# Kernel tuning notes

Hardware: AMD Instinct MI355X
Metric: run time of the kernel (lower is better)

The kernel has to match this reference:

```python
import jax, jax.numpy as jnp
import numpy as np

N_RNA, N_DIS = 50000, 2000
E_RD = E_DR = E_RR = 200000
D_IN, D_DIS, C, H = 256, 128, 64, 4
HC = H * C  # heads * out_channels = 256
NEG_SLOPE = 0.2


def setup_inputs() -> dict:
    ks = jax.random.split(jax.random.key(0), 64)
    it = iter(range(64))
    def nrm(shape, s=0.05):
        return jax.random.normal(ks[next(it)], shape, jnp.float32) * s
    inp = {}
    inp["x_rna"] = nrm((N_RNA, D_IN), 1.0)
    inp["x_dis"] = nrm((N_DIS, D_DIS), 1.0)
    inp["w_rd"] = jax.random.uniform(ks[next(it)], (E_RD,), jnp.float32)
    inp["w_dr"] = jax.random.uniform(ks[next(it)], (E_DR,), jnp.float32)
    inp["w_rr"] = jax.random.uniform(ks[next(it)], (E_RR,), jnp.float32)
    inp["lin_d_W"] = nrm((D_DIS, D_IN)); inp["lin_d_b"] = nrm((D_IN,))
    for rel in ("rd", "dr", "rr"):
        inp[f"{rel}_Wl"]  = nrm((D_IN, HC))   # GATv2 lin_l (source)
        inp[f"{rel}_bl"]  = nrm((HC,))
        inp[f"{rel}_Wr"]  = nrm((D_IN, HC))   # GATv2 lin_r (target)
        inp[f"{rel}_br"]  = nrm((HC,))
        inp[f"{rel}_We"]  = nrm((1, HC))      # lin_edge (edge_dim=1, no bias)
        inp[f"{rel}_att"] = nrm((H, C))       # attention vector per head
        inp[f"{rel}_bias"] = nrm((HC,))       # conv output bias (concat heads)
    inp["lin_out_W"] = nrm((HC, C)); inp["lin_out_b"] = nrm((C,))
    inp["ei_rd_src"] = jax.random.randint(ks[next(it)], (E_RD,), 0, N_RNA)
    inp["ei_rd_dst"] = jax.random.randint(ks[next(it)], (E_RD,), 0, N_DIS)
    inp["ei_dr_src"] = jax.random.randint(ks[next(it)], (E_DR,), 0, N_DIS)
    inp["ei_dr_dst"] = jax.random.randint(ks[next(it)], (E_DR,), 0, N_RNA)
    inp["ei_rr_src"] = jax.random.randint(ks[next(it)], (E_RR,), 0, N_RNA)
    inp["ei_rr_dst"] = jax.random.randint(ks[next(it)], (E_RR,), 0, N_RNA)
    return inp


def _gatv2(x_src, x_dst, src, dst, w, Wl, bl, Wr, br, We, att, bias, n_dst):
    """GATv2Conv with edge_dim=1, add_self_loops=False, concat heads."""
    xl = (x_src @ Wl + bl).reshape(-1, H, C)              # [Ns,H,C]
    xr = (x_dst @ Wr + br).reshape(-1, H, C)              # [Nd,H,C]
    ew = (w[:, None] @ We).reshape(-1, H, C)              # [E,H,C]
    m = jax.nn.leaky_relu(xl[src] + xr[dst] + ew, NEG_SLOPE)
    alpha = jnp.einsum('ehc,hc->eh', m, att)              # [E,H]
    # segment softmax over edges sharing the same destination node
    amax = jax.ops.segment_max(alpha, dst, num_segments=n_dst)
    ex = jnp.exp(alpha - jax.lax.stop_gradient(amax)[dst])
    den = jax.ops.segment_sum(ex, dst, num_segments=n_dst)
    a = ex / (den[dst] + 1e-16)                           # [E,H]
    out = jax.ops.segment_sum(xl[src] * a[..., None], dst, num_segments=n_dst)
    return out.reshape(n_dst, HC) + bias                  # [n_dst, H*C]


def reference(x_rna, x_dis, w_rd, w_dr, w_rr, lin_d_W, lin_d_b,
              rd_Wl, rd_bl, rd_Wr, rd_br, rd_We, rd_att, rd_bias,
              dr_Wl, dr_bl, dr_Wr, dr_br, dr_We, dr_att, dr_bias,
              rr_Wl, rr_bl, rr_Wr, rr_br, rr_We, rr_att, rr_bias,
              lin_out_W, lin_out_b,
              ei_rd_src, ei_rd_dst, ei_dr_src, ei_dr_dst, ei_rr_src, ei_rr_dst):
    xd = x_dis @ lin_d_W + lin_d_b  # project disease feats to rna_in_dim
    h_dis = _gatv2(x_rna, xd, ei_rd_src, ei_rd_dst, w_rd,
                   rd_Wl, rd_bl, rd_Wr, rd_br, rd_We, rd_att, rd_bias, N_DIS)
    h_rna = (_gatv2(xd, x_rna, ei_dr_src, ei_dr_dst, w_dr,
                    dr_Wl, dr_bl, dr_Wr, dr_br, dr_We, dr_att, dr_bias, N_RNA)
             + _gatv2(x_rna, x_rna, ei_rr_src, ei_rr_dst, w_rr,
                      rr_Wl, rr_bl, rr_Wr, rr_br, rr_We, rr_att, rr_bias, N_RNA))
    h_rna = h_rna @ lin_out_W + lin_out_b
    h_dis = h_dis @ lin_out_W + lin_out_b
    return jnp.concatenate([h_rna, h_dis], axis=0)  # [N_RNA+N_DIS, C]
```

## Files before the change

kernel.cpp:

```cpp
#include <hip/hip_runtime.h>
#include <stdint.h>

#define NRNA 50000
#define NDIS 2000
#define NEDGE 200000
#define MP_RNA 50048
#define MP_DIS 2048
#define NOUT 52000
#define MP_OUT2 52096
#define SSTRIDE 50064

#define MAXD0 192
#define MAXD12 32
#define EPB0 0
#define EPB1 (NDIS * MAXD0)
#define EPB2 (EPB1 + NRNA * MAXD12)
#define EPTOT (EPB2 + NRNA * MAXD12)

#define GB_BIG 391
#define GB_SML 16
#define NFILL ((3 * NEDGE + 511) / 512)
#define SWZP 997LL

typedef __attribute__((ext_vector_type(4))) float f32x4;
typedef __attribute__((ext_vector_type(2))) float f32x2;
typedef __attribute__((ext_vector_type(8))) short s16x8;
typedef __attribute__((ext_vector_type(4))) unsigned short u16x4;

#define AS1C const __attribute__((address_space(1))) unsigned int*
#define AS3P __attribute__((address_space(3))) unsigned int*

static __device__ __forceinline__ unsigned short f2b(float f) {
  unsigned u = __float_as_uint(f);
  u += 0x7FFFu + ((u >> 16) & 1u);
  return (unsigned short)(u >> 16);
}
static __device__ __forceinline__ float b2f(unsigned short h) {
  return __uint_as_float(((unsigned)h) << 16);
}
static __device__ __forceinline__ f32x2 unpk2(unsigned u) {
  f32x2 r;
  r[0] = __uint_as_float(u << 16);
  r[1] = __uint_as_float(u & 0xFFFF0000u);
  return r;
}
static __device__ __forceinline__ f32x2 vabs2(f32x2 v) {
  f32x2 r;
  r[0] = __uint_as_float(__float_as_uint(v[0]) & 0x7FFFFFFFu);
  r[1] = __uint_as_float(__float_as_uint(v[1]) & 0x7FFFFFFFu);
  return r;
}

struct TcEnt { const float* W; unsigned short* WT; int K; int N; };
struct Prep {
  const float* xr; unsigned short* xrb;
  const float* xd; unsigned short* xdb;
  TcEnt tc[8];
};
#define PREP_C1 12512
#define PREP_C2 (PREP_C1 + 256)
__global__ __launch_bounds__(256) void k_prep(Prep pr) {
  int id = blockIdx.x;
  if (id < PREP_C1) {
    int idx = (id * 256 + threadIdx.x) * 4;
    int row = idx >> 8;
    u16x4 o;
    if (row < NRNA) {
      f32x4 v = *(const f32x4*)(pr.xr + idx);
      o[0] = f2b(v[0]); o[1] = f2b(v[1]); o[2] = f2b(v[2]); o[3] = f2b(v[3]);
    } else { o[0] = 0; o[1] = 0; o[2] = 0; o[3] = 0; }
    *(u16x4*)(pr.xrb + idx) = o;
  } else if (id < PREP_C2) {
    int idx = ((id - PREP_C1) * 256 + threadIdx.x) * 4;
    int row = idx >> 7;
    u16x4 o;
    if (row < NDIS) {
      f32x4 v = *(const f32x4*)(pr.xd + idx);
      o[0] = f2b(v[0]); o[1] = f2b(v[1]); o[2] = f2b(v[2]); o[3] = f2b(v[3]);
    } else { o[0] = 0; o[1] = 0; o[2] = 0; o[3] = 0; }
    *(u16x4*)(pr.xdb + idx) = o;
  } else {
    int e = (id - PREP_C2) >> 8;
    int idx = ((id - PREP_C2) & 255) * 256 + threadIdx.x;
    TcEnt t = pr.tc[e];
    if (idx < t.K * t.N) {
      int k = idx / t.N, n = idx - k * t.N;
      t.WT[n * t.K + k] = f2b(t.W[idx]);
    }
  }
}

template<int K, int N>
__global__ __launch_bounds__(256) void k_gemm(
    const unsigned short* __restrict__ A, const unsigned short* __restrict__ WT,
    const float* __restrict__ bias, unsigned short* __restrict__ Cb) {
  constexpr int NT = N / 16;
  int lane = threadIdx.x & 63;
  int wave = threadIdx.x >> 6;
  int row0 = blockIdx.x * 64 + wave * 16;
  int lr = lane & 15, kg = lane >> 4;
  f32x4 acc[NT];
#pragma unroll
  for (int i = 0; i < NT; i++) acc[i] = (f32x4)0.f;
  const unsigned short* arow = A + (size_t)(row0 + lr) * K + kg * 8;
#pragma unroll
  for (int kk = 0; kk < K; kk += 32) {
    s16x8 af = *(const s16x8*)(arow + kk);
#pragma unroll
    for (int nt = 0; nt < NT; nt++) {
      s16x8 bf = *(const s16x8*)(WT + (size_t)(nt * 16 + lr) * K + kk + kg * 8);
      acc[nt] = __builtin_amdgcn_mfma_f32_16x16x32_bf16(af, bf, acc[nt], 0, 0, 0);
    }
  }
#pragma unroll
  for (int nt = 0; nt < NT; nt++) {
    int col = nt * 16 + lr;
    float bb = bias[col];
#pragma unroll
    for (int r = 0; r < 4; r++) {
      int row = row0 + kg * 4 + r;
      Cb[(size_t)row * N + col] = f2b(acc[nt][r] + bb);
    }
  }
}

__device__ __forceinline__ void gemm256(const unsigned short* __restrict__ A,
    const unsigned short* __restrict__ WT, const float* __restrict__ bias,
    unsigned short* __restrict__ C, int bxx) {
  __shared__ unsigned short Alds[2][128 * 32];
  __shared__ unsigned short Blds[2][256 * 32];
  const int t = threadIdx.x;
  const int wid = t >> 6, lane = t & 63;
  const int lr = lane & 15, kg = lane >> 4;
  const int wr = wid & 3, wc = wid >> 2;
  const int r0 = bxx * 128;
  f32x4 acc[2][8];
#pragma unroll
  for (int a = 0; a < 2; a++)
#pragma unroll
    for (int b = 0; b < 8; b++) acc[a][b] = (f32x4)0.f;

  auto stage = [&](int buf, int ks) {
    __builtin_amdgcn_global_load_lds(
        (AS1C)(A + (size_t)(r0 + (t & 127)) * 256 + ks * 32 + (t >> 7) * 8),
        (AS3P)((char*)&Alds[buf][0] + t * 16), 16, 0, 0);
    __builtin_amdgcn_global_load_lds(
        (AS1C)(WT + (size_t)(t & 255) * 256 + ks * 32 + (t >> 8) * 8),
        (AS3P)((char*)&Blds[buf][0] + t * 16), 16, 0, 0);
    __builtin_amdgcn_global_load_lds(
        (AS1C)(WT + (size_t)(t & 255) * 256 + ks * 32 + ((t >> 8) + 2) * 8),
        (AS3P)((char*)&Blds[buf][0] + (t + 512) * 16), 16, 0, 0);
  };

  stage(0, 0);
  __syncthreads();
  for (int ks = 0; ks < 8; ++ks) {
    int cur = ks & 1;
    if (ks < 7) stage(cur ^ 1, ks + 1);
    s16x8 a0 = *(const s16x8*)&Alds[cur][(kg * 128 + wr * 32 + lr) * 8];
    s16x8 a1 = *(const s16x8*)&Alds[cur][(kg * 128 + wr * 32 + 16 + lr) * 8];
#pragma unroll
    for (int nt = 0; nt < 8; ++nt) {
      s16x8 bf = *(const s16x8*)&Blds[cur][(kg * 256 + wc * 128 + nt * 16 + lr) * 8];
      acc[0][nt] = __builtin_amdgcn_mfma_f32_16x16x32_bf16(a0, bf, acc[0][nt], 0, 0, 0);
      acc[1][nt] = __builtin_amdgcn_mfma_f32_16x16x32_bf16(a1, bf, acc[1][nt], 0, 0, 0);
    }
    __syncthreads();
  }
#pragma unroll
  for (int nt = 0; nt < 8; ++nt) {
    int col = wc * 128 + nt * 16 + lr;
    float bb = bias[col];
#pragma unroll
    for (int rt = 0; rt < 2; ++rt)
#pragma unroll
      for (int i = 0; i < 4; ++i) {
        int row = r0 + wr * 32 + rt * 16 + kg * 4 + i;
        C[(size_t)row * 256 + col] = f2b(acc[rt][nt][i] + bb);
      }
  }
}

struct MegaG {
  const unsigned short* A[6];
  const unsigned short* WT[6];
  const float* bias[6];
  unsigned short* C[6];
  int off[7];
  int nmega;
  const int* src[3]; const int* dst[3]; const float* w[3];
  int* cnt; unsigned* ep;
};
__global__ __launch_bounds__(512) void k_megaG(MegaG m) {
  int id = (int)(((long long)blockIdx.x * SWZP) % m.nmega);
  if (id < m.off[6]) {
    int sel = 0;
#pragma unroll
    for (int s = 1; s < 6; ++s) sel += (id >= m.off[s]);
    gemm256(m.A[sel], m.WT[sel], m.bias[sel], m.C[sel], id - m.off[sel]);
  } else {
    int i = (id - m.off[6]) * 512 + threadIdx.x;
    if (i < 3 * NEDGE) {
      int r = i / NEDGE;
      int e = i - r * NEDGE;
      int n = m.dst[r][e];
      int c = atomicAdd(&m.cnt[r * SSTRIDE + n], 1);
      int maxd = (r == 0) ? MAXD0 : MAXD12;
      int base = (r == 0) ? EPB0 : (r == 1) ? EPB1 : EPB2;
      if (c < maxd) {
        unsigned v = ((unsigned)f2b(m.w[r][e]) << 16) | (unsigned)m.src[r][e];
        m.ep[base + n * maxd + c] = v;
      }
    }
  }
}

struct G2S { const unsigned short* A; const unsigned short* WT[2];
             const float* b[2]; unsigned short* C[2]; };
__global__ __launch_bounds__(512) void k_gemmP(G2S g) {
  gemm256(g.A, g.WT[blockIdx.y], g.b[blockIdx.y], g.C[blockIdx.y], blockIdx.x);
}

__global__ __launch_bounds__(256) void k_gemmO(const unsigned short* __restrict__ A,
    const unsigned short* __restrict__ WT, const float* __restrict__ bias,
    float* __restrict__ Cf, int Mstore) {
  __shared__ unsigned short Alds[2][128 * 32];
  __shared__ unsigned short Blds[2][64 * 32];
  const int t = threadIdx.x;
  const int lane = t & 63, wid = t >> 6;
  const int lr = lane & 15, kg = lane >> 4;
  const int wr = wid;
  const int r0 = blockIdx.x * 128;
  f32x4 acc[2][4];
#pragma unroll
  for (int a = 0; a < 2; a++)
#pragma unroll
    for (int b = 0; b < 4; b++) acc[a][b] = (f32x4)0.f;
  auto stage = [&](int buf, int ks) {
    __builtin_amdgcn_global_load_lds(
        (AS1C)(A + (size_t)(r0 + (t & 127)) * 256 + ks * 32 + (t >> 7) * 8),
        (AS3P)((char*)&Alds[buf][0] + t * 16), 16, 0, 0);
    __builtin_amdgcn_global_load_lds(
        (AS1C)(A + (size_t)(r0 + (t & 127)) * 256 + ks * 32 + ((t >> 7) + 2) * 8),
        (AS3P)((char*)&Alds[buf][0] + (t + 256) * 16), 16, 0, 0);
    __builtin_amdgcn_global_load_lds(
        (AS1C)(WT + (size_t)(t & 63) * 256 + ks * 32 + (t >> 6) * 8),
        (AS3P)((char*)&Blds[buf][0] + t * 16), 16, 0, 0);
  };
  stage(0, 0);
  __syncthreads();
  for (int ks = 0; ks < 8; ++ks) {
    int cur = ks & 1;
    if (ks < 7) stage(cur ^ 1, ks + 1);
    s16x8 a0 = *(const s16x8*)&Alds[cur][(kg * 128 + wr * 32 + lr) * 8];
    s16x8 a1 = *(const s16x8*)&Alds[cur][(kg * 128 + wr * 32 + 16 + lr) * 8];
#pragma unroll
    for (int nt = 0; nt < 4; ++nt) {
      s16x8 bf = *(const s16x8*)&Blds[cur][(kg * 64 + nt * 16 + lr) * 8];
      acc[0][nt] = __builtin_amdgcn_mfma_f32_16x16x32_bf16(a0, bf, acc[0][nt], 0, 0, 0);
      acc[1][nt] = __builtin_amdgcn_mfma_f32_16x16x32_bf16(a1, bf, acc[1][nt], 0, 0, 0);
    }
    __syncthreads();
  }
#pragma unroll
  for (int nt = 0; nt < 4; ++nt) {
    int col = nt * 16 + lr;
    float bb = bias[col];
#pragma unroll
    for (int rt = 0; rt < 2; ++rt)
#pragma unroll
      for (int i = 0; i < 4; ++i) {
        int row = r0 + wr * 32 + rt * 16 + kg * 4 + i;
        if (row < Mstore) Cf[(size_t)row * 64 + col] = acc[rt][nt][i] + bb;
      }
  }
}

struct Agg {
  f32x2 we01, we23, a6_01, a4_01, a6_23, a4_23, xr01, xr23;
  const unsigned short* xlb;
  const unsigned* epn;
  float m, d;
  f32x2 o01, o23;

  __device__ __forceinline__ void init(const unsigned short* xl, const unsigned short* xr,
      const unsigned* ep_rel, int maxd, int node,
      const float* We, const float* att, int lane) {
    const f32x2* Wep = (const f32x2*)(We + lane * 4);
    we01 = Wep[0]; we23 = Wep[1];
    const f32x2* atp = (const f32x2*)(att + lane * 4);
    a6_01 = atp[0] * 0.6f; a4_01 = atp[0] * 0.4f;
    a6_23 = atp[1] * 0.6f; a4_23 = atp[1] * 0.4f;
    uint2 xruu = *(const uint2*)(xr + (size_t)node * 256 + lane * 4);
    xr01 = unpk2(xruu.x); xr23 = unpk2(xruu.y);
    xlb = xl + lane * 4;
    epn = ep_rel + node * maxd;
    m = -INFINITY; d = 0.f;
    o01 = (f32x2){0.f, 0.f}; o23 = (f32x2){0.f, 0.f};
  }

  __device__ __forceinline__ void batch4(int e, int deg) {
    int nb = deg - e; nb = (nb > 4) ? 4 : nb;
    uint4 pva = *(const uint4*)(epn + e);
    unsigned pv[4] = {pva.x, pva.y, pva.z, pva.w};
    uint2 xv[4];
#pragma unroll
    for (int j = 0; j < 4; j++) {
      unsigned s = (j < nb) ? (pv[j] & 0xFFFFu) : 0u;
      xv[j] = *(const uint2*)(xlb + (s << 8));
    }
    f32x2 x01[4], x23[4];
    float pp[4];
#pragma unroll
    for (int j = 0; j < 4; j++) {
      x01[j] = unpk2(xv[j].x);
      x23[j] = unpk2(xv[j].y);
      float w = __uint_as_float(pv[j] & 0xFFFF0000u);
      f32x2 wv = {w, w};
      f32x2 t01 = (x01[j] + xr01) + wv * we01;
      f32x2 t23 = (x23[j] + xr23) + wv * we23;
      f32x2 q2 = t01 * a6_01;
      q2 = q2 + vabs2(t01) * a4_01;
      q2 = q2 + t23 * a6_23;
      q2 = q2 + vabs2(t23) * a4_23;
      float q = q2[0] + q2[1];
      q += __shfl_xor(q, 1);
      q += __shfl_xor(q, 2);
      q += __shfl_xor(q, 4);
      q += __shfl_xor(q, 8);
      pp[j] = (j < nb) ? q : -INFINITY;
    }
    float mb = fmaxf(fmaxf(pp[0], pp[1]), fmaxf(pp[2], pp[3]));
    float mn = fmaxf(m, mb);
    float sc = __expf(m - mn);
    f32x2 sc2 = {sc, sc};
    d *= sc; o01 *= sc2; o23 *= sc2;
    m = mn;
#pragma unroll
    for (int j = 0; j < 4; j++) {
      float ee = __expf(pp[j] - m);
      f32x2 ee2 = {ee, ee};
      d += ee;
      o01 = o01 + ee2 * x01[j];
      o23 = o23 + ee2 * x23[j];
    }
  }

  __device__ __forceinline__ void finish(float* out) {
    float inv = 1.f / (d + 1e-16f);
    out[0] = o01[0] * inv; out[1] = o01[1] * inv;
    out[2] = o23[0] * inv; out[3] = o23[1] * inv;
  }
};

__device__ __forceinline__ void edge_aggr8(const unsigned short* __restrict__ xl,
    const unsigned short* __restrict__ xr, int deg, const unsigned* __restrict__ ep,
    int maxd, int node, const float* __restrict__ We, const float* __restrict__ att,
    int lane, float* out) {
  const f32x2* Wep = (const f32x2*)(We + lane * 4);
  f32x2 we01 = Wep[0], we23 = Wep[1];
  const f32x2* atp = (const f32x2*)(att + lane * 4);
  f32x2 a6_01 = atp[0] * 0.6f, a4_01 = atp[0] * 0.4f;
  f32x2 a6_23 = atp[1] * 0.6f, a4_23 = atp[1] * 0.4f;
  uint2 xruu = *(const uint2*)(xr + (size_t)node * 256 + lane * 4);
  f32x2 xr01 = unpk2(xruu.x), xr23 = unpk2(xruu.y);
  const unsigned short* xlb = xl + lane * 4;
  float m = -INFINITY, d = 0.f;
  f32x2 o01 = {0.f, 0.f}, o23 = {0.f, 0.f};
  int e0 = node * maxd, e1 = e0 + deg;
  for (int e = e0; e < e1; e += 8) {
    int nb = e1 - e; nb = (nb > 8) ? 8 : nb;
    uint4 pva = *(const uint4*)(ep + e);
    uint4 pvb = *(const uint4*)(ep + e + 4);
    unsigned pv[8] = {pva.x, pva.y, pva.z, pva.w, pvb.x, pvb.y, pvb.z, pvb.w};
    uint2 xv[8];
#pragma unroll
    for (int j = 0; j < 8; j++) {
      unsigned s = (j < nb) ? (pv[j] & 0xFFFFu) : 0u;
      xv[j] = *(const uint2*)(xlb + (s << 8));
    }
    f32x2 x01[8], x23[8];
    float pp[8];
#pragma unroll
    for (int j = 0; j < 8; j++) {
      x01[j] = unpk2(xv[j].x);
      x23[j] = unpk2(xv[j].y);
      float w = __uint_as_float(pv[j] & 0xFFFF0000u);
      f32x2 wv = {w, w};
      f32x2 t01 = (x01[j] + xr01) + wv * we01;
      f32x2 t23 = (x23[j] + xr23) + wv * we23;
      f32x2 q2 = t01 * a6_01;
      q2 = q2 + vabs2(t01) * a4_01;
      q2 = q2 + t23 * a6_23;
      q2 = q2 + vabs2(t23) * a4_23;
      float q = q2[0] + q2[1];
      q += __shfl_xor(q, 1);
      q += __shfl_xor(q, 2);
      q += __shfl_xor(q, 4);
      q += __shfl_xor(q, 8);
      pp[j] = (j < nb) ? q : -INFINITY;
    }
    float mb = fmaxf(fmaxf(fmaxf(pp[0], pp[1]), fmaxf(pp[2], pp[3])),
                     fmaxf(fmaxf(pp[4], pp[5]), fmaxf(pp[6], pp[7])));
    float mn = fmaxf(m, mb);
    float sc = __expf(m - mn);
    f32x2 sc2 = {sc, sc};
    d *= sc; o01 *= sc2; o23 *= sc2;
    m = mn;
#pragma unroll
    for (int j = 0; j < 8; j++) {
      float ee = __expf(pp[j] - m);
      f32x2 ee2 = {ee, ee};
      d += ee;
      o01 = o01 + ee2 * x01[j];
      o23 = o23 + ee2 * x23[j];
    }
  }
  float inv = 1.f / (d + 1e-16f);
  out[0] = o01[0] * inv; out[1] = o01[1] * inv;
  out[2] = o23[0] * inv; out[3] = o23[1] * inv;
}

struct EF {
  const unsigned short *xl_rd, *xr_rd;
  const unsigned short *xl_dr, *xr_dr;
  const unsigned short *xl_rr, *xr_rr;
  const int* cnt; const unsigned* ep;
  const float *We0, *att0, *We1, *att1, *We2, *att2;
  const float *brd, *bdr, *brr;
  unsigned short* h;
};
__global__ __launch_bounds__(256) void k_edgeFull(EF a) {
  int wid = threadIdx.x >> 6, lane = threadIdx.x & 63;
  if (blockIdx.x < NDIS / 4) {
    int node = blockIdx.x * 4 + wid;
    int deg = a.cnt[node]; if (deg > MAXD0) deg = MAXD0;
    float o[4];
    edge_aggr8(a.xl_rd, a.xr_rd, deg, a.ep + EPB0, MAXD0, node, a.We0, a.att0, lane, o);
    f32x4 bb = *(const f32x4*)(a.brd + lane * 4);
    size_t hoff = (size_t)(NRNA + node) * 256 + lane * 4;
    u16x4 ov;
    ov[0] = f2b(bb[0] + o[0]); ov[1] = f2b(bb[1] + o[1]);
    ov[2] = f2b(bb[2] + o[2]); ov[3] = f2b(bb[3] + o[3]);
    *(u16x4*)(a.h + hoff) = ov;
  } else {
    int node = (blockIdx.x - NDIS / 4) * 4 + wid;
    int d1 = a.cnt[SSTRIDE + node]; if (d1 > MAXD12) d1 = MAXD12;
    int d2 = a.cnt[2 * SSTRIDE + node]; if (d2 > MAXD12) d2 = MAXD12;
    Agg A, B;
    A.init(a.xl_dr, a.xr_dr, a.ep + EPB1, MAXD12, node, a.We1, a.att1, lane);
    B.init(a.xl_rr, a.xr_rr, a.ep + EPB2, MAXD12, node, a.We2, a.att2, lane);
    int nb1 = (d1 + 3) >> 2, nb2 = (d2 + 3) >> 2;
    int nmn = (nb1 < nb2) ? nb1 : nb2;
    int i = 0;
    for (; i < nmn; ++i) { A.batch4(i * 4, d1); B.batch4(i * 4, d2); }
    for (; i < nb1; ++i) A.batch4(i * 4, d1);
    for (; i < nb2; ++i) B.batch4(i * 4, d2);
    float o1[4], o2[4];
    A.finish(o1); B.finish(o2);
    f32x4 b1 = *(const f32x4*)(a.bdr + lane * 4);
    f32x4 b2 = *(const f32x4*)(a.brr + lane * 4);
    size_t hoff = (size_t)node * 256 + lane * 4;
    u16x4 ov;
    ov[0] = f2b(b1[0] + b2[0] + o1[0] + o2[0]);
    ov[1] = f2b(b1[1] + b2[1] + o1[1] + o2[1]);
    ov[2] = f2b(b1[2] + b2[2] + o1[2] + o2[2]);
    ov[3] = f2b(b1[3] + b2[3] + o1[3] + o2[3]);
    *(u16x4*)(a.h + hoff) = ov;
  }
}

struct EA2 {
  const unsigned short *xl0, *xr0, *xl1, *xr1;
  const int* cnt; const unsigned* ep;
  const float *We0, *att0, *We1, *att1;
  const float *brd, *bdr, *brr;
  unsigned short* h;
};
__global__ __launch_bounds__(256) void k_edgeAB2(EA2 a) {
  int wid = threadIdx.x >> 6, lane = threadIdx.x & 63;
  float o[4];
  size_t hoff;
  f32x4 bb;
  if (blockIdx.x < NDIS / 4) {
    int node = blockIdx.x * 4 + wid;
    int deg = a.cnt[node]; if (deg > MAXD0) deg = MAXD0;
    edge_aggr8(a.xl0, a.xr0, deg, a.ep + EPB0, MAXD0, node, a.We0, a.att0, lane, o);
    f32x4 b0 = *(const f32x4*)(a.brd + lane * 4);
    bb = b0;
    hoff = (size_t)(NRNA + node) * 256 + lane * 4;
  } else {
    int node = (blockIdx.x - NDIS / 4) * 4 + wid;
    int deg = a.cnt[SSTRIDE + node]; if (deg > MAXD12) deg = MAXD12;
    Agg A;
    A.init(a.xl1, a.xr1, a.ep + EPB1, MAXD12, node, a.We1, a.att1, lane);
    int nb = (deg + 3) >> 2;
    for (int i = 0; i < nb; ++i) A.batch4(i * 4, deg);
    A.finish(o);
    f32x4 b1 = *(const f32x4*)(a.bdr + lane * 4);
    f32x4 b2 = *(const f32x4*)(a.brr + lane * 4);
    bb[0] = b1[0] + b2[0]; bb[1] = b1[1] + b2[1];
    bb[2] = b1[2] + b2[2]; bb[3] = b1[3] + b2[3];
    hoff = (size_t)node * 256 + lane * 4;
  }
  u16x4 ov;
  ov[0] = f2b(bb[0] + o[0]); ov[1] = f2b(bb[1] + o[1]);
  ov[2] = f2b(bb[2] + o[2]); ov[3] = f2b(bb[3] + o[3]);
  *(u16x4*)(a.h + hoff) = ov;
}

__global__ __launch_bounds__(256) void k_edgeRR(
    const unsigned short* __restrict__ xl, const unsigned short* __restrict__ xr,
    const int* __restrict__ cnt, const unsigned* __restrict__ epr,
    const float* __restrict__ We, const float* __restrict__ att,
    unsigned short* __restrict__ h) {
  int wid = threadIdx.x >> 6, lane = threadIdx.x & 63;
  int node = blockIdx.x * 4 + wid;
  int deg = cnt[node]; if (deg > MAXD12) deg = MAXD12;
  float o[4];
  Agg A;
  A.init(xl, xr, epr, MAXD12, node, We, att, lane);
  int nb = (deg + 3) >> 2;
  for (int i = 0; i < nb; ++i) A.batch4(i * 4, deg);
  A.finish(o);
  size_t hoff = (size_t)node * 256 + lane * 4;
  u16x4 hp = *(const u16x4*)(h + hoff);
  u16x4 ov;
  ov[0] = f2b(b2f(hp[0]) + o[0]);
  ov[1] = f2b(b2f(hp[1]) + o[1]);
  ov[2] = f2b(b2f(hp[2]) + o[2]);
  ov[3] = f2b(b2f(hp[3]) + o[3]);
  *(u16x4*)(h + hoff) = ov;
}

extern "C" void kernel_launch(void* const* d_in, const int* in_sizes, int n_in,
                              void* d_out, int out_size, void* d_ws, size_t ws_size,
                              hipStream_t stream) {
  (void)in_sizes; (void)n_in; (void)out_size;
  const float* x_rna = (const float*)d_in[0];
  const float* x_dis = (const float*)d_in[1];
  const float* wedge[3] = {(const float*)d_in[2], (const float*)d_in[3], (const float*)d_in[4]};
  const float* lin_d_W = (const float*)d_in[5];
  const float* lin_d_b = (const float*)d_in[6];
  const float *Wl[3], *bl[3], *Wr[3], *br[3], *We[3], *att[3], *bias[3];
  for (int r = 0; r < 3; r++) {
    const int base = 7 + r * 7;
    Wl[r]   = (const float*)d_in[base + 0];
    bl[r]   = (const float*)d_in[base + 1];
    Wr[r]   = (const float*)d_in[base + 2];
    br[r]   = (const float*)d_in[base + 3];
    We[r]   = (const float*)d_in[base + 4];
    att[r]  = (const float*)d_in[base + 5];
    bias[r] = (const float*)d_in[base + 6];
  }
  const float* lin_out_W = (const float*)d_in[28];
  const float* lin_out_b = (const float*)d_in[29];
  const int* esrc_in[3] = {(const int*)d_in[30], (const int*)d_in[32], (const int*)d_in[34]};
  const int* edst_in[3] = {(const int*)d_in[31], (const int*)d_in[33], (const int*)d_in[35]};

  char* p = (char*)d_ws;
  auto alloc = [&](size_t b) -> void* {
    void* r = (void*)p;
    p += (b + 511) & ~(size_t)511;
    return r;
  };
  const size_t BIGB = ((size_t)MP_RNA * 256 * 2 + 511) & ~(size_t)511;
  unsigned short* xrna_b = (unsigned short*)alloc((size_t)MP_RNA * 256 * 2);
  unsigned short* xdis_b = (unsigned short*)alloc((size_t)MP_DIS * 128 * 2);
  unsigned short* xd_b   = (unsigned short*)alloc((size_t)MP_DIS * 256 * 2);
  unsigned short* wt_lind = (unsigned short*)alloc(256 * 128 * 2);
  unsigned short *wt_l[3], *wt_r[3];
  for (int r = 0; r < 3; r++) {
    wt_l[r] = (unsigned short*)alloc(256 * 256 * 2);
    wt_r[r] = (unsigned short*)alloc(256 * 256 * 2);
  }
  unsigned short* wt_out = (unsigned short*)alloc(64 * 256 * 2);
  unsigned short* big1   = (unsigned short*)alloc((size_t)MP_RNA * 256 * 2);
  unsigned short* big2   = (unsigned short*)alloc((size_t)MP_RNA * 256 * 2);
  unsigned short* small1 = (unsigned short*)alloc((size_t)MP_DIS * 256 * 2);
  unsigned short* small2 = (unsigned short*)alloc((size_t)MP_DIS * 256 * 2);
  unsigned short* h_b    = (unsigned short*)alloc((size_t)MP_OUT2 * 256 * 2);
  int*      cnt = (int*)alloc((size_t)3 * SSTRIDE * 4);
  unsigned* ep  = (unsigned*)alloc((size_t)EPTOT * 4 + 64);
  if ((size_t)(p - (char*)d_ws) > ws_size) return;

  bool pathA = ((size_t)(p - (char*)d_ws) + 2 * BIGB) <= ws_size;
  unsigned short* big3 = nullptr;
  unsigned short* big4 = nullptr;
  if (pathA) {
    big3 = (unsigned short*)alloc((size_t)MP_RNA * 256 * 2);
    big4 = (unsigned short*)alloc((size_t)MP_RNA * 256 * 2);
  }

  hipMemsetAsync(cnt, 0, (size_t)3 * SSTRIDE * 4, stream);

  Prep pr;
  pr.xr = x_rna; pr.xrb = xrna_b; pr.xd = x_dis; pr.xdb = xdis_b;
  pr.tc[0] = {lin_d_W, wt_lind, 128, 256};
  for (int r = 0; r < 3; r++) {
    pr.tc[1 + 2 * r] = {Wl[r], wt_l[r], 256, 256};
    pr.tc[2 + 2 * r] = {Wr[r], wt_r[r], 256, 256};
  }
  pr.tc[7] = {lin_out_W, wt_out, 256, 64};
  k_prep<<<PREP_C2 + 8 * 256, 256, 0, stream>>>(pr);

  k_gemm<128, 256><<<MP_DIS / 64, 256, 0, stream>>>(xdis_b, wt_lind, lin_d_b, xd_b);

  MegaG m;
  for (int r = 0; r < 3; r++) { m.src[r] = esrc_in[r]; m.dst[r] = edst_in[r]; m.w[r] = wedge[r]; }
  m.cnt = cnt; m.ep = ep;

  if (pathA) {
    m.A[0] = xrna_b; m.A[1] = xrna_b; m.A[2] = xrna_b; m.A[3] = xrna_b;
    m.A[4] = xd_b;   m.A[5] = xd_b;
    m.WT[0] = wt_l[0]; m.WT[1] = wt_r[1]; m.WT[2] = wt_l[2]; m.WT[3] = wt_r[2];
    m.WT[4] = wt_r[0]; m.WT[5] = wt_l[1];
    m.bias[0] = bl[0]; m.bias[1] = br[1]; m.bias[2] = bl[2]; m.bias[3] = br[2];
    m.bias[4] = br[0]; m.bias[5] = bl[1];
    m.C[0] = big1; m.C[1] = big2; m.C[2] = big3; m.C[3] = big4;
    m.C[4] = small1; m.C[5] = small2;
    m.off[0] = 0; m.off[1] = GB_BIG; m.off[2] = 2 * GB_BIG; m.off[3] = 3 * GB_BIG;
    m.off[4] = 4 * GB_BIG; m.off[5] = 4 * GB_BIG + GB_SML; m.off[6] = 4 * GB_BIG + 2 * GB_SML;
    m.nmega = m.off[6] + NFILL;
    k_megaG<<<m.nmega, 512, 0, stream>>>(m);

    EF ef = {big1, small1, small2, big2, big3, big4, cnt, ep,
             We[0], att[0], We[1], att[1], We[2], att[2],
             bias[0], bias[1], bias[2], h_b};
    k_edgeFull<<<NDIS / 4 + NRNA / 4, 256, 0, stream>>>(ef);
  } else {
    m.A[0] = xrna_b; m.A[1] = xrna_b; m.A[2] = xd_b; m.A[3] = xd_b;
    m.A[4] = xd_b;   m.A[5] = xd_b;
    m.WT[0] = wt_l[0]; m.WT[1] = wt_r[1]; m.WT[2] = wt_r[0]; m.WT[3] = wt_l[1];
    m.WT[4] = wt_r[0]; m.WT[5] = wt_l[1];
    m.bias[0] = bl[0]; m.bias[1] = br[1]; m.bias[2] = br[0]; m.bias[3] = bl[1];
    m.bias[4] = br[0]; m.bias[5] = bl[1];
    m.C[0] = big1; m.C[1] = big2; m.C[2] = small1; m.C[3] = small2;
    m.C[4] = small1; m.C[5] = small2;
    m.off[0] = 0; m.off[1] = GB_BIG; m.off[2] = 2 * GB_BIG;
    m.off[3] = 2 * GB_BIG + GB_SML; m.off[4] = 2 * GB_BIG + 2 * GB_SML;
    m.off[5] = m.off[4]; m.off[6] = m.off[4];
    m.nmega = m.off[6] + NFILL;
    k_megaG<<<m.nmega, 512, 0, stream>>>(m);

    EA2 a = {big1, small1, small2, big2, cnt, ep,
             We[0], att[0], We[1], att[1],
             bias[0], bias[1], bias[2], h_b};
    k_edgeAB2<<<NDIS / 4 + NRNA / 4, 256, 0, stream>>>(a);

    G2S g = {xrna_b, {wt_l[2], wt_r[2]}, {bl[2], br[2]}, {big1, big2}};
    k_gemmP<<<dim3(GB_BIG, 2), 512, 0, stream>>>(g);

    k_edgeRR<<<NRNA / 4, 256, 0, stream>>>(big1, big2, cnt + 2 * SSTRIDE, ep + EPB2,
                                           We[2], att[2], h_b);
  }

  k_gemmO<<<MP_OUT2 / 128, 256, 0, stream>>>(h_b, wt_out, lin_out_b, (float*)d_out, NOUT);
}
```

Before: 230.6 us.

## Split dr and rr aggregations of each RNA node across separate wavefronts

The edge-aggregation kernel now uses 512-thread blocks. Each RNA node's dr and rr relation aggregations run on two different wavefronts instead of being interleaved in a single wavefront. The rr partial result goes through shared memory, and the dr wave combines both and writes the output. Disease blocks now handle 8 nodes each. This doubles wavefront-level parallelism for the RNA side and shortens each wave's serial chain, at the cost of a block-wide barrier, LDS traffic, and wave imbalance when the two degrees differ.

Measured after the change: 249.5 us. 8.2% more time.

```diff
diff --git a/kernel.cpp b/kernel.cpp
--- a/kernel.cpp
+++ b/kernel.cpp
@@ -21,6 +21,9 @@
 #define GB_SML 16
 #define NFILL ((3 * NEDGE + 511) / 512)
 #define SWZP 997LL
+
+#define EDGE_DIS_BLKS (NDIS / 8)
+#define EDGE_RNA_BLKS (NRNA / 4)
 
 typedef __attribute__((ext_vector_type(4))) float f32x4;
 typedef __attribute__((ext_vector_type(2))) float f32x2;
@@ -430,10 +433,10 @@
   const float *brd, *bdr, *brr;
   unsigned short* h;
 };
-__global__ __launch_bounds__(256) void k_edgeFull(EF a) {
+__global__ __launch_bounds__(512) void k_edgeFull(EF a) {
   int wid = threadIdx.x >> 6, lane = threadIdx.x & 63;
-  if (blockIdx.x < NDIS / 4) {
-    int node = blockIdx.x * 4 + wid;
+  if (blockIdx.x < EDGE_DIS_BLKS) {
+    int node = blockIdx.x * 8 + wid;
     int deg = a.cnt[node]; if (deg > MAXD0) deg = MAXD0;
     float o[4];
     edge_aggr8(a.xl_rd, a.xr_rd, deg, a.ep + EPB0, MAXD0, node, a.We0, a.att0, lane, o);
@@ -444,29 +447,35 @@
     ov[2] = f2b(bb[2] + o[2]); ov[3] = f2b(bb[3] + o[3]);
     *(u16x4*)(a.h + hoff) = ov;
   } else {
-    int node = (blockIdx.x - NDIS / 4) * 4 + wid;
-    int d1 = a.cnt[SSTRIDE + node]; if (d1 > MAXD12) d1 = MAXD12;
-    int d2 = a.cnt[2 * SSTRIDE + node]; if (d2 > MAXD12) d2 = MAXD12;
-    Agg A, B;
-    A.init(a.xl_dr, a.xr_dr, a.ep + EPB1, MAXD12, node, a.We1, a.att1, lane);
-    B.init(a.xl_rr, a.xr_rr, a.ep + EPB2, MAXD12, node, a.We2, a.att2, lane);
-    int nb1 = (d1 + 3) >> 2, nb2 = (d2 + 3) >> 2;
-    int nmn = (nb1 < nb2) ? nb1 : nb2;
-    int i = 0;
-    for (; i < nmn; ++i) { A.batch4(i * 4, d1); B.batch4(i * 4, d2); }
-    for (; i < nb1; ++i) A.batch4(i * 4, d1);
-    for (; i < nb2; ++i) B.batch4(i * 4, d2);
-    float o1[4], o2[4];
-    A.finish(o1); B.finish(o2);
-    f32x4 b1 = *(const f32x4*)(a.bdr + lane * 4);
-    f32x4 b2 = *(const f32x4*)(a.brr + lane * 4);
-    size_t hoff = (size_t)node * 256 + lane * 4;
-    u16x4 ov;
-    ov[0] = f2b(b1[0] + b2[0] + o1[0] + o2[0]);
-    ov[1] = f2b(b1[1] + b2[1] + o1[1] + o2[1]);
-    ov[2] = f2b(b1[2] + b2[2] + o1[2] + o2[2]);
-    ov[3] = f2b(b1[3] + b2[3] + o1[3] + o2[3]);
-    *(u16x4*)(a.h + hoff) = ov;
+    __shared__ float ls[4][64][4];
+    int node = (blockIdx.x - EDGE_DIS_BLKS) * 4 + (wid & 3);
+    bool isRR = wid >= 4;
+    int deg = a.cnt[(isRR ? 2 : 1) * SSTRIDE + node];
+    if (deg > MAXD12) deg = MAXD12;
+    Agg A;
+    A.init(isRR ? a.xl_rr : a.xl_dr, isRR ? a.xr_rr : a.xr_dr,
+           a.ep + (isRR ? EPB2 : EPB1), MAXD12, node,
+           isRR ? a.We2 : a.We1, isRR ? a.att2 : a.att1, lane);
+    int nb = (deg + 3) >> 2;
+    for (int i = 0; i < nb; ++i) A.batch4(i * 4, deg);
+    float o[4];
+    A.finish(o);
+    if (isRR) {
+      ls[wid - 4][lane][0] = o[0]; ls[wid - 4][lane][1] = o[1];
+      ls[wid - 4][lane][2] = o[2]; ls[wid - 4][lane][3] = o[3];
+    }
+    __syncthreads();
+    if (!isRR) {
+      f32x4 b1 = *(const f32x4*)(a.bdr + lane * 4);
+      f32x4 b2 = *(const f32x4*)(a.brr + lane * 4);
+      size_t hoff = (size_t)node * 256 + lane * 4;
+      u16x4 ov;
+      ov[0] = f2b(b1[0] + b2[0] + o[0] + ls[wid][lane][0]);
+      ov[1] = f2b(b1[1] + b2[1] + o[1] + ls[wid][lane][1]);
+      ov[2] = f2b(b1[2] + b2[2] + o[2] + ls[wid][lane][2]);
+      ov[3] = f2b(b1[3] + b2[3] + o[3] + ls[wid][lane][3]);
+      *(u16x4*)(a.h + hoff) = ov;
+    }
   }
 }
 
@@ -627,7 +636,7 @@
     EF ef = {big1, small1, small2, big2, big3, big4, cnt, ep,
              We[0], att[0], We[1], att[1], We[2], att[2],
              bias[0], bias[1], bias[2], h_b};
-    k_edgeFull<<<NDIS / 4 + NRNA / 4, 256, 0, stream>>>(ef);
+    k_edgeFull<<<EDGE_DIS_BLKS + EDGE_RNA_BLKS, 512, 0, stream>>>(ef);
   } else {
     m.A[0] = xrna_b; m.A[1] = xrna_b; m.A[2] = xd_b; m.A[3] = xd_b;
     m.A[4] = xd_b;   m.A[5] = xd_b;
```
